# Kernel tuning notes

Measured on AMD Instinct MI355X. Metric: run time of the kernel, lower is better.

Reference implementation:

```python
import jax, jax.numpy as jnp
import numpy as np

H = 65  # LSTM units / vocab size
L = 3   # stacked layers (shared weights)

def _lstm_step(x, h, c, W, U, b):
    # Keras LSTMCell gate order: i, f, c(bar), o
    z = x @ W + h @ U + b  # [B, 4H]
    i, f, g, o = jnp.split(z, 4, axis=-1)
    i = jax.nn.sigmoid(i)
    f = jax.nn.sigmoid(f)
    g = jnp.tanh(g)
    o = jax.nn.sigmoid(o)
    c_new = f * c + i * g
    h_new = o * jnp.tanh(c_new)
    return h_new, c_new

def setup_inputs() -> dict:
    key = jax.random.key(0)
    ks = jax.random.split(key, 4)
    B, T = 50, 4096
    x = jax.random.normal(ks[0], (B, T, H), dtype=jnp.float32)
    s = 1.0 / np.sqrt(H)
    W = jax.random.normal(ks[1], (H, 4 * H), dtype=jnp.float32) * s
    U = jax.random.normal(ks[2], (H, 4 * H), dtype=jnp.float32) * s
    b = jnp.zeros((4 * H,), dtype=jnp.float32)
    Wd = jax.random.normal(ks[3], (H, H), dtype=jnp.float32) * s
    bd = jnp.zeros((H,), dtype=jnp.float32)
    return {"x": x, "W": W, "U": U, "b": b, "Wd": Wd, "bd": bd}

def reference(x, W, U, b, Wd, bd):
    B, T, _ = x.shape
    h0 = jnp.zeros((L, B, H), dtype=x.dtype)
    c0 = jnp.zeros((L, B, H), dtype=x.dtype)

    def step(carry, x_t):
        h, c = carry  # each [L, B, H]
        inp = x_t
        hs, cs = [], []
        for l in range(L):  # 3 layers, SAME weights (shared cell object)
            h_l, c_l = _lstm_step(inp, h[l], c[l], W, U, b)
            hs.append(h_l)
            cs.append(c_l)
            inp = h_l
        return (jnp.stack(hs), jnp.stack(cs)), inp  # output = top-layer hidden

    _, ys = jax.lax.scan(step, (h0, c0), jnp.swapaxes(x, 0, 1))  # ys: [T, B, H]
    ys = jnp.swapaxes(ys, 0, 1)  # [B, T, H]
    return ys @ Wd + bd
```

## Files before the change

kernel.cpp:

```cpp
#include <hip/hip_runtime.h>


#define HH    65
#define G4    260
#define TT    4096
#define NB    50
#define BLOCK 512
#define DROWS 64

#define KEEP4(v) asm volatile("" : "+v"(v.x), "+v"(v.y), "+v"(v.z), "+v"(v.w))
#define KEEP(s)  asm volatile("" : "+v"(s))

__device__ __forceinline__ float sigm(float x)  { return 1.0f / (1.0f + __expf(-x)); }
__device__ __forceinline__ float tanha(float x) { float e = __expf(2.0f * x); return 1.0f - 2.0f / (e + 1.0f); }

__device__ __forceinline__ float qsum(float v) {
    int i = __float_as_int(v);
    v += __int_as_float(__builtin_amdgcn_update_dpp(0, i, 0xB1, 0xF, 0xF, true));
    i = __float_as_int(v);
    v += __int_as_float(__builtin_amdgcn_update_dpp(0, i, 0x4E, 0xF, 0xF, true));
    return v;
}

__global__ void __launch_bounds__(BLOCK)
__attribute__((amdgpu_waves_per_eu(2, 2)))
charrnn_rec(const float* __restrict__ x, const float* __restrict__ W,
            const float* __restrict__ U, const float* __restrict__ bv,
            float* __restrict__ out)
{
    __shared__ __align__(16) float s_hin[3][68];
    __shared__ __align__(16) float s_hrec[3][68];
    __shared__ __align__(16) float s_z[3][2][256];
    __shared__ float s_parte[3][2][4];

    const int bat = blockIdx.x;
    const int tid = threadIdx.x;
    const float* xb   = x   + (size_t)bat * TT * HH;
    float*       outb = out + (size_t)bat * TT * HH;

    for (int i = tid; i < 3 * 68; i += BLOCK) { (&s_hin[0][0])[i] = 0.0f; (&s_hrec[0][0])[i] = 0.0f; }

    const int w    = tid & 3;
    const int side = tid >> 8;
    const int qL   = (tid >> 2) & 63;
    const int col0 = qL * 4;
    const float* M = side ? U : W;

    float4 wa0, wa1, wa2, wa3, wb0, wb1, wb2, wb3,
           wc0, wc1, wc2, wc3, wd0, wd1, wd2, wd3;
#define WLD(v, c, q)                                                          \
    do {                                                                      \
        v.x = M[(16 * w + 4 * (q) + 0) * G4 + col0 + (c)];                    \
        v.y = M[(16 * w + 4 * (q) + 1) * G4 + col0 + (c)];                    \
        v.z = M[(16 * w + 4 * (q) + 2) * G4 + col0 + (c)];                    \
        v.w = M[(16 * w + 4 * (q) + 3) * G4 + col0 + (c)];                    \
        KEEP4(v);                                                             \
    } while (0)
    WLD(wa0, 0, 0); WLD(wa1, 0, 1); WLD(wa2, 0, 2); WLD(wa3, 0, 3);
    WLD(wb0, 1, 0); WLD(wb1, 1, 1); WLD(wb2, 1, 2); WLD(wb3, 1, 3);
    WLD(wc0, 2, 0); WLD(wc1, 2, 1); WLD(wc2, 2, 2); WLD(wc3, 2, 3);
    WLD(wd0, 3, 0); WLD(wd1, 3, 1); WLD(wd2, 3, 2); WLD(wd3, 3, 3);
#undef WLD
    float ws0 = (w == 3) ? M[64 * G4 + col0 + 0] : 0.0f; KEEP(ws0);
    float ws1 = (w == 3) ? M[64 * G4 + col0 + 1] : 0.0f; KEEP(ws1);
    float ws2 = (w == 3) ? M[64 * G4 + col0 + 2] : 0.0f; KEEP(ws2);
    float ws3 = (w == 3) ? M[64 * G4 + col0 + 3] : 0.0f; KEEP(ws3);

    const bool isX  = ((tid & 255) < 16);
    const int  colX = 256 + ((tid >> 2) & 3);
    float4 e0, e1, e2, e3;
    float  esc;
#define ELD(v, q)                                                             \
    do {                                                                      \
        v.x = isX ? M[(16 * w + 4 * (q) + 0) * G4 + colX] : 0.0f;             \
        v.y = isX ? M[(16 * w + 4 * (q) + 1) * G4 + colX] : 0.0f;             \
        v.z = isX ? M[(16 * w + 4 * (q) + 2) * G4 + colX] : 0.0f;             \
        v.w = isX ? M[(16 * w + 4 * (q) + 3) * G4 + colX] : 0.0f;             \
        KEEP4(v);                                                             \
    } while (0)
    ELD(e0, 0); ELD(e1, 1); ELD(e2, 2); ELD(e3, 3);
#undef ELD
    esc = (isX && w == 3) ? M[64 * G4 + colX] : 0.0f; KEEP(esc);

    const int  cl = tid / 65, n = tid - (tid / 65) * 65;
    const bool isC = (tid < 195);
    const float bz0 = bv[n], bz1 = bv[65 + n], bz2 = bv[130 + n], bz3 = bv[195 + n];
    float creg = 0.0f;

    const bool isP  = (tid >= 447);
    const int  pidx = tid - 447;
    float cur = 0.0f, nxt = 0.0f;
    if (isP) {
        s_hin[0][pidx] = xb[pidx];
        cur = xb[HH + pidx];
    }
    __syncthreads();

    for (int r = 0; r < TT + 2; ++r) {
        if (isP) {
            const int tn = r + 2;
            nxt = (tn < TT) ? xb[(size_t)tn * HH + pidx] : 0.0f;
        }
#pragma unroll
        for (int l = 0; l < 3; ++l) {
            if ((unsigned)(r - l) < TT) {
                const float* hb = side ? &s_hrec[l][0] : &s_hin[l][0];
                const float4* h4 = (const float4*)(hb + 16 * w);
                const float4 H0 = h4[0], H1 = h4[1], H2 = h4[2], H3 = h4[3];
                const float  h64 = hb[64];
                float a0, a1, a2, a3;
#define COLDOT(acc, p0, p1, p2, p3, ps)                                       \
    {   float u0, u1;                                                         \
        u0 = H0.x * p0.x;           u1 = H0.y * p0.y;                         \
        u0 = fmaf(H0.z, p0.z, u0);  u1 = fmaf(H0.w, p0.w, u1);                \
        u0 = fmaf(H1.x, p1.x, u0);  u1 = fmaf(H1.y, p1.y, u1);                \
        u0 = fmaf(H1.z, p1.z, u0);  u1 = fmaf(H1.w, p1.w, u1);                \
        u0 = fmaf(H2.x, p2.x, u0);  u1 = fmaf(H2.y, p2.y, u1);                \
        u0 = fmaf(H2.z, p2.z, u0);  u1 = fmaf(H2.w, p2.w, u1);                \
        u0 = fmaf(H3.x, p3.x, u0);  u1 = fmaf(H3.y, p3.y, u1);                \
        u0 = fmaf(H3.z, p3.z, u0);  u1 = fmaf(H3.w, p3.w, u1);                \
        u0 = fmaf(h64, ps, u0);                                               \
        acc = u0 + u1; }
                COLDOT(a0, wa0, wa1, wa2, wa3, ws0)
                COLDOT(a1, wb0, wb1, wb2, wb3, ws1)
                COLDOT(a2, wc0, wc1, wc2, wc3, ws2)
                COLDOT(a3, wd0, wd1, wd2, wd3, ws3)
                a0 = qsum(a0); a1 = qsum(a1); a2 = qsum(a2); a3 = qsum(a3);
                if (w == 0)
                    *(float4*)&s_z[l][side][col0] = make_float4(a0, a1, a2, a3);
                if (isX) {
                    float ea;
                    COLDOT(ea, e0, e1, e2, e3, esc)
                    ea = qsum(ea);
                    if (w == 0) s_parte[l][side][(tid >> 2) & 3] = ea;
                }
#undef COLDOT
            }
        }
        __syncthreads();

        if (isC) {
            if ((unsigned)(r - cl) < TT) {
                const float zi = bz0 + s_z[cl][0][n]       + s_z[cl][1][n];
                const float zf = bz1 + s_z[cl][0][65 + n]  + s_z[cl][1][65 + n];
                const float zg = bz2 + s_z[cl][0][130 + n] + s_z[cl][1][130 + n];
                float zo;
                if (n < 61) zo = bz3 + s_z[cl][0][195 + n]   + s_z[cl][1][195 + n];
                else        zo = bz3 + s_parte[cl][0][n - 61] + s_parte[cl][1][n - 61];
                const float ig = sigm(zi), fg = sigm(zf), gg = tanha(zg), og = sigm(zo);
                creg = fmaf(fg, creg, ig * gg);
                const float h = og * tanha(creg);
                s_hrec[cl][n] = h;
                if (cl < 2) s_hin[cl + 1][n] = h;
                else        outb[(size_t)(r - cl) * HH + n] = h;
            }
        }
        if (isP) {
            if (r + 1 < TT) s_hin[0][pidx] = cur;
            cur = nxt;
        }
        __syncthreads();
    }
}

__global__ void __launch_bounds__(256, 1)
dense_head(float* __restrict__ io, const float* __restrict__ Wd, const float* __restrict__ bd)
{
    __shared__ __align__(16) float s_h[DROWS][68];
    __shared__ float s_wd[HH][HH];
    __shared__ float s_bd[HH];

    const int tid = threadIdx.x;
    float* base = io + (size_t)blockIdx.x * DROWS * HH;

    for (int i = tid; i < DROWS * HH; i += 256) {
        const int row = i / HH, k = i - row * HH;
        s_h[row][k] = base[i];
    }
    for (int i = tid; i < HH * HH; i += 256) (&s_wd[0][0])[i] = Wd[i];
    if (tid < HH) s_bd[tid] = bd[tid];
    __syncthreads();

    for (int u = tid; u < DROWS * HH; u += 256) {
        const int row = u / HH, c = u - row * HH;
        const float4* hp = (const float4*)&s_h[row][0];
        float acc = s_bd[c];
#pragma unroll
        for (int k4 = 0; k4 < 16; ++k4) {
            const float4 hv = hp[k4];
            acc = fmaf(hv.x, s_wd[4 * k4 + 0][c], acc);
            acc = fmaf(hv.y, s_wd[4 * k4 + 1][c], acc);
            acc = fmaf(hv.z, s_wd[4 * k4 + 2][c], acc);
            acc = fmaf(hv.w, s_wd[4 * k4 + 3][c], acc);
        }
        acc = fmaf(s_h[row][64], s_wd[64][c], acc);
        base[u] = acc;
    }
}

extern "C" void kernel_launch(void* const* d_in, const int* in_sizes, int n_in,
                              void* d_out, int out_size, void* d_ws, size_t ws_size,
                              hipStream_t stream)
{
    const float* x  = (const float*)d_in[0];
    const float* W  = (const float*)d_in[1];
    const float* U  = (const float*)d_in[2];
    const float* bv = (const float*)d_in[3];
    const float* Wd = (const float*)d_in[4];
    const float* bd = (const float*)d_in[5];
    float* out = (float*)d_out;

    hipLaunchKernelGGL(charrnn_rec, dim3(NB), dim3(BLOCK), 0, stream, x, W, U, bv, out);
    hipLaunchKernelGGL(dense_head, dim3(NB * TT / DROWS), dim3(256), 0, stream, out, Wd, bd);
}
```

Measured before the change: 6.013 ms.

## Add dedicated waves for extra gate columns, cell updates and input prefetch

Grows the block from 512 to 768 threads. The 512 gate threads now only compute the main 256-column dot products. The added four waves take the leftover 4 columns, the three layers' cell updates (one wave per layer, plus stragglers for unit 64) and the x prefetch. This removes the divergent extra-column work from the gate waves and spreads the elementwise LSTM update across waves, so each per-step critical section is shorter. In exchange there are more waves at each barrier, and waves_per_eu rises to 3, which may tighten the register budget for the 68-register weight cache.

```diff
diff --git a/kernel.cpp b/kernel.cpp
--- a/kernel.cpp
+++ b/kernel.cpp
@@ -5,7 +5,8 @@
 #define G4    260
 #define TT    4096
 #define NB    50
-#define BLOCK 512
+#define BLOCK 768
+#define NGATE 512
 #define DROWS 64
 
 #define KEEP4(v) asm volatile("" : "+v"(v.x), "+v"(v.y), "+v"(v.z), "+v"(v.w))
@@ -23,7 +24,7 @@
 }
 
 __global__ void __launch_bounds__(BLOCK)
-__attribute__((amdgpu_waves_per_eu(2, 2)))
+__attribute__((amdgpu_waves_per_eu(3, 3)))
 charrnn_rec(const float* __restrict__ x, const float* __restrict__ W,
             const float* __restrict__ U, const float* __restrict__ bv,
             float* __restrict__ out)
@@ -40,20 +41,24 @@
 
     for (int i = tid; i < 3 * 68; i += BLOCK) { (&s_hin[0][0])[i] = 0.0f; (&s_hrec[0][0])[i] = 0.0f; }
 
+    const bool isG  = (tid < NGATE);
+    const int  atid = tid - NGATE;
+    const int  awv  = (atid >> 6) & 3;
+    const int  al   = atid & 63;
+
     const int w    = tid & 3;
     const int side = tid >> 8;
-    const int qL   = (tid >> 2) & 63;
-    const int col0 = qL * 4;
+    const int col0 = ((tid >> 2) & 63) * 4;
     const float* M = side ? U : W;
 
     float4 wa0, wa1, wa2, wa3, wb0, wb1, wb2, wb3,
            wc0, wc1, wc2, wc3, wd0, wd1, wd2, wd3;
 #define WLD(v, c, q)                                                          \
     do {                                                                      \
-        v.x = M[(16 * w + 4 * (q) + 0) * G4 + col0 + (c)];                    \
-        v.y = M[(16 * w + 4 * (q) + 1) * G4 + col0 + (c)];                    \
-        v.z = M[(16 * w + 4 * (q) + 2) * G4 + col0 + (c)];                    \
-        v.w = M[(16 * w + 4 * (q) + 3) * G4 + col0 + (c)];                    \
+        v.x = isG ? M[(16 * w + 4 * (q) + 0) * G4 + col0 + (c)] : 0.0f;       \
+        v.y = isG ? M[(16 * w + 4 * (q) + 1) * G4 + col0 + (c)] : 0.0f;       \
+        v.z = isG ? M[(16 * w + 4 * (q) + 2) * G4 + col0 + (c)] : 0.0f;       \
+        v.w = isG ? M[(16 * w + 4 * (q) + 3) * G4 + col0 + (c)] : 0.0f;       \
         KEEP4(v);                                                             \
     } while (0)
     WLD(wa0, 0, 0); WLD(wa1, 0, 1); WLD(wa2, 0, 2); WLD(wa3, 0, 3);
@@ -61,54 +66,66 @@
     WLD(wc0, 2, 0); WLD(wc1, 2, 1); WLD(wc2, 2, 2); WLD(wc3, 2, 3);
     WLD(wd0, 3, 0); WLD(wd1, 3, 1); WLD(wd2, 3, 2); WLD(wd3, 3, 3);
 #undef WLD
-    float ws0 = (w == 3) ? M[64 * G4 + col0 + 0] : 0.0f; KEEP(ws0);
-    float ws1 = (w == 3) ? M[64 * G4 + col0 + 1] : 0.0f; KEEP(ws1);
-    float ws2 = (w == 3) ? M[64 * G4 + col0 + 2] : 0.0f; KEEP(ws2);
-    float ws3 = (w == 3) ? M[64 * G4 + col0 + 3] : 0.0f; KEEP(ws3);
-
-    const bool isX  = ((tid & 255) < 16);
-    const int  colX = 256 + ((tid >> 2) & 3);
+    float ws0 = (isG && w == 3) ? M[64 * G4 + col0 + 0] : 0.0f; KEEP(ws0);
+    float ws1 = (isG && w == 3) ? M[64 * G4 + col0 + 1] : 0.0f; KEEP(ws1);
+    float ws2 = (isG && w == 3) ? M[64 * G4 + col0 + 2] : 0.0f; KEEP(ws2);
+    float ws3 = (isG && w == 3) ? M[64 * G4 + col0 + 3] : 0.0f; KEEP(ws3);
+
+    const bool isE = (!isG) && (al < 8);
+    const int  es  = (al >> 2) & 1;
+    const int  ew  = al & 3;
+    const int  colE = 256 + awv;
+    const float* ME = es ? U : W;
     float4 e0, e1, e2, e3;
-    float  esc;
 #define ELD(v, q)                                                             \
     do {                                                                      \
-        v.x = isX ? M[(16 * w + 4 * (q) + 0) * G4 + colX] : 0.0f;             \
-        v.y = isX ? M[(16 * w + 4 * (q) + 1) * G4 + colX] : 0.0f;             \
-        v.z = isX ? M[(16 * w + 4 * (q) + 2) * G4 + colX] : 0.0f;             \
-        v.w = isX ? M[(16 * w + 4 * (q) + 3) * G4 + colX] : 0.0f;             \
+        v.x = isE ? ME[(16 * ew + 4 * (q) + 0) * G4 + colE] : 0.0f;           \
+        v.y = isE ? ME[(16 * ew + 4 * (q) + 1) * G4 + colE] : 0.0f;           \
+        v.z = isE ? ME[(16 * ew + 4 * (q) + 2) * G4 + colE] : 0.0f;           \
+        v.w = isE ? ME[(16 * ew + 4 * (q) + 3) * G4 + colE] : 0.0f;           \
         KEEP4(v);                                                             \
     } while (0)
     ELD(e0, 0); ELD(e1, 1); ELD(e2, 2); ELD(e3, 3);
 #undef ELD
-    esc = (isX && w == 3) ? M[64 * G4 + colX] : 0.0f; KEEP(esc);
-
-    const int  cl = tid / 65, n = tid - (tid / 65) * 65;
-    const bool isC = (tid < 195);
-    const float bz0 = bv[n], bz1 = bv[65 + n], bz2 = bv[130 + n], bz3 = bv[195 + n];
+    float esc = (isE && ew == 3) ? ME[64 * G4 + colE] : 0.0f; KEEP(esc);
+
+    const bool isB  = (!isG) && (awv < 3);
+    const bool isB64 = (!isG) && (awv == 3) && (al < 3);
+    const int  cl = isB ? awv : (isB64 ? al : 0);
+    const int  cn = isB ? al : 64;
+    const bool anyB = isB || isB64;
+    const float bz0 = anyB ? bv[cn]       : 0.0f;
+    const float bz1 = anyB ? bv[65 + cn]  : 0.0f;
+    const float bz2 = anyB ? bv[130 + cn] : 0.0f;
+    const float bz3 = anyB ? bv[195 + cn] : 0.0f;
     float creg = 0.0f;
 
-    const bool isP  = (tid >= 447);
-    const int  pidx = tid - 447;
-    float cur = 0.0f, nxt = 0.0f;
+    const bool isP  = (!isG) && (awv == 3);
+    const bool isP2 = isP && (al == 63);
+    const int  pidx = al;
+    float cur0 = 0.0f, nxt0 = 0.0f, cur1 = 0.0f, nxt1 = 0.0f;
     if (isP) {
         s_hin[0][pidx] = xb[pidx];
-        cur = xb[HH + pidx];
+        cur0 = xb[HH + pidx];
+        if (isP2) { s_hin[0][64] = xb[64]; cur1 = xb[HH + 64]; }
     }
     __syncthreads();
 
     for (int r = 0; r < TT + 2; ++r) {
         if (isP) {
             const int tn = r + 2;
-            nxt = (tn < TT) ? xb[(size_t)tn * HH + pidx] : 0.0f;
-        }
+            nxt0 = (tn < TT) ? xb[(size_t)tn * HH + pidx] : 0.0f;
+            if (isP2) nxt1 = (tn < TT) ? xb[(size_t)tn * HH + 64] : 0.0f;
+        }
+        if (isG) {
 #pragma unroll
-        for (int l = 0; l < 3; ++l) {
-            if ((unsigned)(r - l) < TT) {
-                const float* hb = side ? &s_hrec[l][0] : &s_hin[l][0];
-                const float4* h4 = (const float4*)(hb + 16 * w);
-                const float4 H0 = h4[0], H1 = h4[1], H2 = h4[2], H3 = h4[3];
-                const float  h64 = hb[64];
-                float a0, a1, a2, a3;
+            for (int l = 0; l < 3; ++l) {
+                if ((unsigned)(r - l) < TT) {
+                    const float* hb = side ? &s_hrec[l][0] : &s_hin[l][0];
+                    const float4* h4 = (const float4*)(hb + 16 * w);
+                    const float4 H0 = h4[0], H1 = h4[1], H2 = h4[2], H3 = h4[3];
+                    const float  h64 = hb[64];
+                    float a0, a1, a2, a3;
 #define COLDOT(acc, p0, p1, p2, p3, ps)                                       \
     {   float u0, u1;                                                         \
         u0 = H0.x * p0.x;           u1 = H0.y * p0.y;                         \
@@ -121,43 +138,55 @@
         u0 = fmaf(H3.z, p3.z, u0);  u1 = fmaf(H3.w, p3.w, u1);                \
         u0 = fmaf(h64, ps, u0);                                               \
         acc = u0 + u1; }
-                COLDOT(a0, wa0, wa1, wa2, wa3, ws0)
-                COLDOT(a1, wb0, wb1, wb2, wb3, ws1)
-                COLDOT(a2, wc0, wc1, wc2, wc3, ws2)
-                COLDOT(a3, wd0, wd1, wd2, wd3, ws3)
-                a0 = qsum(a0); a1 = qsum(a1); a2 = qsum(a2); a3 = qsum(a3);
-                if (w == 0)
-                    *(float4*)&s_z[l][side][col0] = make_float4(a0, a1, a2, a3);
-                if (isX) {
+                    COLDOT(a0, wa0, wa1, wa2, wa3, ws0)
+                    COLDOT(a1, wb0, wb1, wb2, wb3, ws1)
+                    COLDOT(a2, wc0, wc1, wc2, wc3, ws2)
+                    COLDOT(a3, wd0, wd1, wd2, wd3, ws3)
+                    a0 = qsum(a0); a1 = qsum(a1); a2 = qsum(a2); a3 = qsum(a3);
+                    if (w == 0)
+                        *(float4*)&s_z[l][side][col0] = make_float4(a0, a1, a2, a3);
+                }
+            }
+        } else if (isE) {
+#pragma unroll
+            for (int l = 0; l < 3; ++l) {
+                if ((unsigned)(r - l) < TT) {
+                    const float* hb = es ? &s_hrec[l][0] : &s_hin[l][0];
+                    const float4* h4 = (const float4*)(hb + 16 * ew);
+                    const float4 H0 = h4[0], H1 = h4[1], H2 = h4[2], H3 = h4[3];
+                    const float  h64 = hb[64];
                     float ea;
                     COLDOT(ea, e0, e1, e2, e3, esc)
                     ea = qsum(ea);
-                    if (w == 0) s_parte[l][side][(tid >> 2) & 3] = ea;
+                    if (ew == 0) s_parte[l][es][awv] = ea;
                 }
+            }
 #undef COLDOT
-            }
         }
         __syncthreads();
 
-        if (isC) {
+        if (anyB) {
             if ((unsigned)(r - cl) < TT) {
-                const float zi = bz0 + s_z[cl][0][n]       + s_z[cl][1][n];
-                const float zf = bz1 + s_z[cl][0][65 + n]  + s_z[cl][1][65 + n];
-                const float zg = bz2 + s_z[cl][0][130 + n] + s_z[cl][1][130 + n];
+                const float zi = bz0 + s_z[cl][0][cn]       + s_z[cl][1][cn];
+                const float zf = bz1 + s_z[cl][0][65 + cn]  + s_z[cl][1][65 + cn];
+                const float zg = bz2 + s_z[cl][0][130 + cn] + s_z[cl][1][130 + cn];
                 float zo;
-                if (n < 61) zo = bz3 + s_z[cl][0][195 + n]   + s_z[cl][1][195 + n];
-                else        zo = bz3 + s_parte[cl][0][n - 61] + s_parte[cl][1][n - 61];
+                if (cn < 61) zo = bz3 + s_z[cl][0][195 + cn]    + s_z[cl][1][195 + cn];
+                else         zo = bz3 + s_parte[cl][0][cn - 61] + s_parte[cl][1][cn - 61];
                 const float ig = sigm(zi), fg = sigm(zf), gg = tanha(zg), og = sigm(zo);
                 creg = fmaf(fg, creg, ig * gg);
                 const float h = og * tanha(creg);
-                s_hrec[cl][n] = h;
-                if (cl < 2) s_hin[cl + 1][n] = h;
-                else        outb[(size_t)(r - cl) * HH + n] = h;
+                s_hrec[cl][cn] = h;
+                if (cl < 2) s_hin[cl + 1][cn] = h;
+                else        outb[(size_t)(r - cl) * HH + cn] = h;
             }
         }
         if (isP) {
-            if (r + 1 < TT) s_hin[0][pidx] = cur;
-            cur = nxt;
+            if (r + 1 < TT) {
+                s_hin[0][pidx] = cur0;
+                if (isP2) s_hin[0][64] = cur1;
+            }
+            cur0 = nxt0; cur1 = nxt1;
         }
         __syncthreads();
     }
```

Result: faster. 5.678 ms (-5.6%).
